# Kernel tuning notes

Hardware: AMD Instinct MI355X
Metric: run time of the kernel (lower is better)

Reference implementation:

```python
import jax, jax.numpy as jnp
import numpy as np

N = 25000      # nodes
E = 400000     # edges (avg degree 16)
MUL = 32       # multiplicity of each irrep block
NSC = 8        # num_edge_scalar_attr
HID = 64       # radial_neurons
WNUM = 4 * MUL # tp.weight_numel (4 uvu paths x mul 32)
NUM_NEIGH = 16.0
INV_SQRT3 = 1.0 / np.sqrt(3.0)   # component-normalized CG for 1o x 1o -> 0e


def setup_inputs() -> dict:
    key = jax.random.key(0)
    ks = jax.random.split(key, 13)
    return {
        'node_input': jax.random.normal(ks[0], (N, 4 * MUL), jnp.float32),
        'node_attr_input': jax.random.normal(ks[1], (N, 1), jnp.float32),
        'node_attr_output': jax.random.normal(ks[2], (N, 1), jnp.float32),
        'edge_src': jax.random.randint(ks[3], (E,), 0, N),
        'edge_dst': jax.random.randint(ks[4], (E,), 0, N),
        'edge_attr': jax.random.normal(ks[5], (E, 4), jnp.float32),
        'edge_scalar_attr': jax.random.normal(ks[6], (E, NSC), jnp.float32),
        # lin1: FCTP(32x0e+32x1o, 1x0e, 32x0e+32x1o) -> two uvw weight blocks (mul2=1 squeezed)
        'w1_s': jax.random.normal(ks[7], (MUL, MUL), jnp.float32),
        'w1_v': jax.random.normal(ks[8], (MUL, MUL), jnp.float32),
        # radial FC net [8, 64, 128]
        'Wfc1': jax.random.normal(ks[9], (NSC, HID), jnp.float32),
        'Wfc2': jax.random.normal(ks[10], (HID, WNUM), jnp.float32),
        # lin2: FCTP(irreps_mid, 1x0e, 32x0e+32x1o): 2 scalar blocks -> 0e, 2 vector blocks -> 1o
        'w2_s': jax.random.normal(ks[11], (2, MUL, MUL), jnp.float32),
        'w2_v': jax.random.normal(ks[12], (2, MUL, MUL), jnp.float32),
    }


def reference(node_input, node_attr_input, node_attr_output, edge_src, edge_dst,
              edge_attr, edge_scalar_attr, w1_s, w1_v, Wfc1, Wfc2, w2_s, w2_v):
    n = node_input.shape[0]
    # split node features into 32x0e scalars and 32x1o vectors
    xs = node_input[:, :MUL]                      # [N, 32]
    xv = node_input[:, MUL:].reshape(n, MUL, 3)   # [N, 32, 3]
    a = node_attr_input[:, 0]                     # [N]

    # ---- lin1: FullyConnectedTensorProduct with 1x0e attr (per-path alpha = 1/sqrt(mul1*mul2))
    inv1 = 1.0 / np.sqrt(MUL * 1.0)
    xs1 = jnp.einsum('nu,n,uw->nw', xs, a, w1_s) * inv1
    xv1 = jnp.einsum('nui,n,uw->nwi', xv, a, w1_v) * inv1

    # ---- radial FC net (silu MLP, fan-in normalized)
    h = jax.nn.silu(edge_scalar_attr @ Wfc1 * (1.0 / np.sqrt(NSC)))
    w = (h @ Wfc2 * (1.0 / np.sqrt(HID))).reshape(-1, 4, MUL)  # [E, 4 paths, 32]

    # ---- gather source node features per edge
    es = xs1[edge_src]            # [E, 32]
    ev = xv1[edge_src]            # [E, 32, 3]
    ys = edge_attr[:, 0]          # [E]    (0e sh)
    yv = edge_attr[:, 1:4]        # [E, 3] (1o sh)

    # ---- CG tensor product, 4 uvu instructions with per-edge weights
    m0 = w[:, 0] * es * ys[:, None]                                   # 0e x 0e -> 0e
    m3 = w[:, 3] * jnp.einsum('eui,ei->eu', ev, yv) * INV_SQRT3       # 1o x 1o -> 0e
    m1 = w[:, 1][:, :, None] * es[:, :, None] * yv[:, None, :]        # 0e x 1o -> 1o
    m2 = w[:, 2][:, :, None] * ev * ys[:, None, None]                 # 1o x 0e -> 1o
    ne = m0.shape[0]
    edge_features = jnp.concatenate(
        [m0, m3, m1.reshape(ne, 3 * MUL), m2.reshape(ne, 3 * MUL)], axis=1)  # [E, 256]

    # ---- scatter-sum to destination nodes, divide by sqrt(num_neighbors)
    mid = jax.ops.segment_sum(edge_features, edge_dst, num_segments=n)
    mid = mid / np.sqrt(NUM_NEIGH)

    # ---- lin2: FCTP(irreps_mid, 1x0e, 32x0e+32x1o), element norm: alpha = 1/sqrt(2*mul)
    b = node_attr_output[:, 0]
    inv2 = 1.0 / np.sqrt(2.0 * MUL)
    s0 = mid[:, :MUL]
    s1 = mid[:, MUL:2 * MUL]
    v1 = mid[:, 2 * MUL:2 * MUL + 3 * MUL].reshape(n, MUL, 3)
    v2 = mid[:, 2 * MUL + 3 * MUL:].reshape(n, MUL, 3)
    out_s = (jnp.einsum('nu,n,uw->nw', s0, b, w2_s[0]) +
             jnp.einsum('nu,n,uw->nw', s1, b, w2_s[1])) * inv2
    out_v = (jnp.einsum('nui,n,uw->nwi', v1, b, w2_v[0]) +
             jnp.einsum('nui,n,uw->nwi', v2, b, w2_v[1])) * inv2
    return jnp.concatenate([out_s, out_v.reshape(n, 3 * MUL)], axis=1)  # [N, 128]
```

## Files before the change

kernel.cpp:

```cpp
#include <hip/hip_runtime.h>


typedef __attribute__((ext_vector_type(8))) short bf16x8;
typedef __attribute__((ext_vector_type(4))) float f32x4;

__device__ __forceinline__ unsigned bf16r(float x) {
    unsigned u = __float_as_uint(x);
    return (u + 0x7fffu + ((u >> 16) & 1u)) >> 16;
}
__device__ __forceinline__ float bflo(unsigned p) { return __uint_as_float(p << 16); }
__device__ __forceinline__ float bfhi(unsigned p) { return __uint_as_float(p & 0xffff0000u); }

__global__ __launch_bounds__(256) void prep_kernel(
    const float* __restrict__ Wfc1, const float* __restrict__ Wfc2,
    float* __restrict__ W1s, float* __restrict__ W2T, unsigned short* __restrict__ W2Tb)
{
    int t = blockIdx.x * 256 + threadIdx.x;
    const float inv_sqrt_nsc = 0.35355339059327373f;
    if (t < 8 * 64) W1s[t] = Wfc1[t] * inv_sqrt_nsc;
    if (t < 64 * 128) {
        int r = t >> 7, c = t & 127;
        float v = Wfc2[t] * 0.125f;
        W2T[c * 64 + r] = v;
        W2Tb[c * 64 + r] = (unsigned short)bf16r(v);
    }
}

__global__ __launch_bounds__(256) void node_in_kernel(
    const float* __restrict__ node_input, const float* __restrict__ attr_in,
    const float* __restrict__ w1s, const float* __restrict__ w1v,
    float* __restrict__ xsv1, int n_nodes)
{
    __shared__ float sWs[1024], sWv[1024], srow[2][128];
    for (int k = threadIdx.x; k < 1024; k += 256) { sWs[k] = w1s[k]; sWv[k] = w1v[k]; }
    int j = threadIdx.x & 127;
    int half = threadIdx.x >> 7;
    int w = 0, i = 0;
    if (j >= 32) { int jj = j - 32; w = jj / 3; i = jj - 3 * w; }
    const float inv1 = 0.17677669529663687f;
    for (int base = blockIdx.x * 2; base < n_nodes; base += gridDim.x * 2) {
        int n = base + half;
        __syncthreads();
        if (n < n_nodes) srow[half][j] = node_input[(size_t)n * 128 + j];
        __syncthreads();
        if (n < n_nodes) {
            float acc = 0.0f;
            if (j < 32) {
                #pragma unroll
                for (int u = 0; u < 32; u++) acc += srow[half][u] * sWs[u * 32 + j];
            } else {
                #pragma unroll
                for (int u = 0; u < 32; u++) acc += srow[half][32 + 3 * u + i] * sWv[u * 32 + w];
            }
            xsv1[(size_t)n * 128 + j] = acc * (attr_in[n] * inv1);
        }
    }
}

__global__ __launch_bounds__(256) void count_kernel(
    const int* __restrict__ edst, int* __restrict__ counts, int n_edges)
{
    int e = blockIdx.x * 256 + threadIdx.x;
    if (e < n_edges) atomicAdd(&counts[edst[e]], 1);
}

__global__ __launch_bounds__(1024) void scan_kernel(
    const int* __restrict__ counts, int* __restrict__ offs, int* __restrict__ cursor, int n)
{
    __shared__ int part[1024];
    int tid = threadIdx.x;
    int chunk = (n + 1023) / 1024;
    int begin = tid * chunk;
    int end = begin + chunk; if (end > n) end = n;
    int s = 0;
    for (int i = begin; i < end; i++) s += counts[i];
    part[tid] = s;
    __syncthreads();
    for (int off = 1; off < 1024; off <<= 1) {
        int v = (tid >= off) ? part[tid - off] : 0;
        __syncthreads();
        part[tid] += v;
        __syncthreads();
    }
    int base = (tid == 0) ? 0 : part[tid - 1];
    for (int i = begin; i < end; i++) {
        offs[i] = base; cursor[i] = base;
        base += counts[i];
    }
    if (tid == 1023) offs[n] = part[1023];
}

__global__ __launch_bounds__(256) void scatter_kernel(
    const int* __restrict__ edst, const int* __restrict__ esrc,
    const float* __restrict__ eattr, const float* __restrict__ escal,
    int* __restrict__ cursor,
    int* __restrict__ esrc_s, float4* __restrict__ eattr_s, float4* __restrict__ escal_s,
    int n_edges)
{
    int e = blockIdx.x * 256 + threadIdx.x;
    if (e < n_edges) {
        int d = edst[e];
        int p = atomicAdd(&cursor[d], 1);
        esrc_s[p] = esrc[e];
        eattr_s[p] = *reinterpret_cast<const float4*>(eattr + (size_t)e * 4);
        escal_s[2 * (size_t)p]     = *reinterpret_cast<const float4*>(escal + (size_t)e * 8);
        escal_s[2 * (size_t)p + 1] = *reinterpret_cast<const float4*>(escal + (size_t)e * 8 + 4);
    }
}

#define TPW 8
__global__ __launch_bounds__(256) void edge_mlp_v4(
    const float4* __restrict__ escal_s,
    const float* __restrict__ W1s, const unsigned short* __restrict__ W2Tb,
    unsigned short* __restrict__ wbuf, int n_edges, int nrt)
{
    int tid = threadIdx.x;
    int wv = tid >> 6, l = tid & 63;
    int lm = l & 15, lk = l >> 4;
    int k0 = lk * 8;
    int rt0 = (blockIdx.x * 4 + wv) * TPW;

    bf16x8 bf[8][2];
    #pragma unroll
    for (int t = 0; t < 8; t++) {
        int n = t * 16 + lm;
        bf[t][0] = *reinterpret_cast<const bf16x8*>(W2Tb + n * 64 + k0);
        bf[t][1] = *reinterpret_cast<const bf16x8*>(W2Tb + n * 64 + k0 + 32);
    }

    #pragma unroll 2
    for (int t8 = 0; t8 < TPW; t8++) {
        int rt = rt0 + t8;
        if (rt >= nrt) break;
        int kidx = rt * 16 + lm;

        float q[8];
        if (kidx < n_edges) {
            float4 qa = escal_s[2 * (size_t)kidx];
            float4 qb = escal_s[2 * (size_t)kidx + 1];
            q[0] = qa.x; q[1] = qa.y; q[2] = qa.z; q[3] = qa.w;
            q[4] = qb.x; q[5] = qb.y; q[6] = qb.z; q[7] = qb.w;
        } else {
            #pragma unroll
            for (int i = 0; i < 8; i++) q[i] = 0.f;
        }

        union Af { bf16x8 v; unsigned u[4]; };
        Af af0, af1;
        #pragma unroll
        for (int half = 0; half < 2; half++) {
            int kb = k0 + half * 32;
            float h[8];
            #pragma unroll
            for (int i = 0; i < 8; i++) h[i] = 0.f;
            #pragma unroll
            for (int in = 0; in < 8; in++) {
                float qi = q[in];
                float4 wa = *reinterpret_cast<const float4*>(W1s + in * 64 + kb);
                float4 wb = *reinterpret_cast<const float4*>(W1s + in * 64 + kb + 4);
                h[0] += qi * wa.x; h[1] += qi * wa.y; h[2] += qi * wa.z; h[3] += qi * wa.w;
                h[4] += qi * wb.x; h[5] += qi * wb.y; h[6] += qi * wb.z; h[7] += qi * wb.w;
            }
            unsigned* dst = half ? af1.u : af0.u;
            #pragma unroll
            for (int p = 0; p < 4; p++) {
                float s0 = h[2 * p], s1 = h[2 * p + 1];
                s0 = s0 / (1.0f + __expf(-s0));
                s1 = s1 / (1.0f + __expf(-s1));
                dst[p] = bf16r(s0) | (bf16r(s1) << 16);
            }
        }

        #pragma unroll
        for (int t = 0; t < 8; t++) {
            f32x4 a4 = {0.f, 0.f, 0.f, 0.f};
            a4 = __builtin_amdgcn_mfma_f32_16x16x32_bf16(af0.v, bf[t][0], a4, 0, 0, 0);
            a4 = __builtin_amdgcn_mfma_f32_16x16x32_bf16(af1.v, bf[t][1], a4, 0, 0, 0);
            unsigned s0 = bf16r(a4[0]) | (bf16r(a4[1]) << 16);
            unsigned s1 = bf16r(a4[2]) | (bf16r(a4[3]) << 16);
            *reinterpret_cast<uint2*>(wbuf + ((size_t)(rt * 8 + t) * 256) + l * 4) = make_uint2(s0, s1);
        }
    }
}

__global__ __launch_bounds__(256) void gather_node_kernel(
    const unsigned short* __restrict__ wbuf, const float* __restrict__ xsv1,
    const int* __restrict__ esrc_s, const float4* __restrict__ eattr_s,
    const int* __restrict__ offs, float* __restrict__ mid, int n_nodes)
{
    int tid = threadIdx.x;
    int wv = __builtin_amdgcn_readfirstlane(tid >> 6);
    int L = tid & 63;
    int n = blockIdx.x * 4 + wv;
    if (n >= n_nodes) return;
    int g = L >> 4;

    int be, fbase; bool six;
    if (g == 0)      { be = 2 * L;       fbase = 2 * L;      six = false; }
    else if (g == 1) { be = 2 * L - 32;  fbase = 6 * L - 32; six = true;  }
    else if (g == 2) { be = 6 * L - 160; fbase = 6 * L - 32; six = true;  }
    else             { be = 6 * L - 256; fbase = 2 * L - 64; six = false; }

    const int colpart = ((2 * L) >> 4) * 256 + (((2 * L) & 15) << 2);

    const float inv_sqrt3 = 0.5773502691896258f;
    float a0 = 0.f, a1 = 0.f, a2 = 0.f, a3 = 0.f, a4 = 0.f, a5 = 0.f;
    int start = offs[n], end = offs[n + 1];

    #pragma unroll 4
    for (int k = start; k < end; k++) {
        float4 ea = eattr_s[k];
        int epart = (k >> 4) * 2048 + (((k >> 2) & 3) << 6);
        int sel = k & 3;
        uint4 wq = *reinterpret_cast<const uint4*>(wbuf + (size_t)epart + colpart);
        unsigned ulo = (sel & 2) ? wq.y : wq.x;
        unsigned uhi = (sel & 2) ? wq.w : wq.z;
        float wlo = (sel & 1) ? bfhi(ulo) : bflo(ulo);
        float whi = (sel & 1) ? bfhi(uhi) : bflo(uhi);
        int src = esrc_s[k];
        const float* __restrict__ nb = xsv1 + (size_t)src * 128;
        if (g == 0) {
            float2 x0 = *reinterpret_cast<const float2*>(nb + be);
            a0 += wlo * x0.x * ea.x;
            a1 += whi * x0.y * ea.x;
        } else if (g == 1) {
            float2 x0 = *reinterpret_cast<const float2*>(nb + be);
            float b0 = wlo * x0.x, b1 = whi * x0.y;
            a0 += b0 * ea.y; a1 += b0 * ea.z; a2 += b0 * ea.w;
            a3 += b1 * ea.y; a4 += b1 * ea.z; a5 += b1 * ea.w;
        } else {
            float2 x0 = *reinterpret_cast<const float2*>(nb + be);
            float2 x1 = *reinterpret_cast<const float2*>(nb + be + 2);
            float2 x2 = *reinterpret_cast<const float2*>(nb + be + 4);
            if (g == 2) {
                float b0 = wlo * ea.x, b1 = whi * ea.x;
                a0 += b0 * x0.x; a1 += b0 * x0.y; a2 += b0 * x1.x;
                a3 += b1 * x1.y; a4 += b1 * x2.x; a5 += b1 * x2.y;
            } else {
                a0 += wlo * (x0.x * ea.y + x0.y * ea.z + x1.x * ea.w) * inv_sqrt3;
                a1 += whi * (x1.y * ea.y + x2.x * ea.z + x2.y * ea.w) * inv_sqrt3;
            }
        }
    }

    float* row = mid + (size_t)n * 256 + fbase;
    *reinterpret_cast<float2*>(row) = make_float2(a0, a1);
    if (six) {
        *reinterpret_cast<float2*>(row + 2) = make_float2(a2, a3);
        *reinterpret_cast<float2*>(row + 4) = make_float2(a4, a5);
    }
}

__global__ __launch_bounds__(256) void edge_kernel_atomic(
    const float* __restrict__ xsv1, const int* __restrict__ esrc, const int* __restrict__ edst,
    const float* __restrict__ eattr, const float* __restrict__ escal,
    const float* __restrict__ W1s, const float* __restrict__ W2T,
    float* __restrict__ mid, int n_edges)
{
    int e = blockIdx.x * 256 + threadIdx.x;
    if (e >= n_edges) return;
    const float4 qa = *reinterpret_cast<const float4*>(escal + (size_t)e * 8);
    const float4 qb = *reinterpret_cast<const float4*>(escal + (size_t)e * 8 + 4);
    float h[64];
    #pragma unroll
    for (int t = 0; t < 64; t++) {
        float acc = qa.x * W1s[t]       + qa.y * W1s[64 + t]
                  + qa.z * W1s[128 + t] + qa.w * W1s[192 + t]
                  + qb.x * W1s[256 + t] + qb.y * W1s[320 + t]
                  + qb.z * W1s[384 + t] + qb.w * W1s[448 + t];
        h[t] = acc / (1.0f + __expf(-acc));
    }
    int src = esrc[e], dst = edst[e];
    const float4 ea = *reinterpret_cast<const float4*>(eattr + (size_t)e * 4);
    const float ys = ea.x, yv0 = ea.y, yv1 = ea.z, yv2 = ea.w;
    const float* __restrict__ nb = xsv1 + (size_t)src * 128;
    float* __restrict__ op = mid + (size_t)dst * 256;
    const float inv_sqrt3 = 0.5773502691896258f;
    for (int u = 0; u < 32; u++) {
        float w0 = 0.f, w1 = 0.f, w2 = 0.f, w3 = 0.f;
        const float* __restrict__ r0 = W2T + (size_t)u * 64;
        const float* __restrict__ r1 = W2T + (size_t)(32 + u) * 64;
        const float* __restrict__ r2 = W2T + (size_t)(64 + u) * 64;
        const float* __restrict__ r3 = W2T + (size_t)(96 + u) * 64;
        #pragma unroll
        for (int t = 0; t < 64; t++) {
            float hv = h[t];
            w0 += hv * r0[t]; w1 += hv * r1[t]; w2 += hv * r2[t]; w3 += hv * r3[t];
        }
        float es  = nb[u];
        float ev0 = nb[32 + 3 * u], ev1 = nb[33 + 3 * u], ev2 = nb[34 + 3 * u];
        atomicAdd(op + u,      w0 * es * ys);
        atomicAdd(op + 32 + u, w3 * (ev0 * yv0 + ev1 * yv1 + ev2 * yv2) * inv_sqrt3);
        float a1 = w1 * es;
        atomicAdd(op + 64 + 3 * u, a1 * yv0);
        atomicAdd(op + 65 + 3 * u, a1 * yv1);
        atomicAdd(op + 66 + 3 * u, a1 * yv2);
        float a2 = w2 * ys;
        atomicAdd(op + 160 + 3 * u, a2 * ev0);
        atomicAdd(op + 161 + 3 * u, a2 * ev1);
        atomicAdd(op + 162 + 3 * u, a2 * ev2);
    }
}

__global__ __launch_bounds__(256) void node_out_kernel(
    const float* __restrict__ mid, const float* __restrict__ attr_out,
    const float* __restrict__ w2s, const float* __restrict__ w2v,
    float* __restrict__ out, int n_nodes)
{
    __shared__ float sS0[1024], sS1[1024], sV0[1024], sV1[1024];
    for (int k = threadIdx.x; k < 1024; k += 256) {
        sS0[k] = w2s[k]; sS1[k] = w2s[1024 + k];
        sV0[k] = w2v[k]; sV1[k] = w2v[1024 + k];
    }
    __syncthreads();
    int j = threadIdx.x & 127;
    int half = threadIdx.x >> 7;
    int w = 0, i = 0;
    if (j >= 32) { int jj = j - 32; w = jj / 3; i = jj - 3 * w; }
    const float scale = 0.125f * 0.25f;
    for (int base = blockIdx.x * 2; base < n_nodes; base += gridDim.x * 2) {
        int n = base + half;
        if (n >= n_nodes) continue;
        const float* __restrict__ mr = mid + (size_t)n * 256;
        float acc = 0.0f;
        if (j < 32) {
            #pragma unroll
            for (int u = 0; u < 32; u++)
                acc += mr[u] * sS0[u * 32 + j] + mr[32 + u] * sS1[u * 32 + j];
        } else {
            #pragma unroll
            for (int u = 0; u < 32; u++)
                acc += mr[64 + 3 * u + i] * sV0[u * 32 + w] + mr[160 + 3 * u + i] * sV1[u * 32 + w];
        }
        out[(size_t)n * 128 + j] = acc * (attr_out[n] * scale);
    }
}

extern "C" void kernel_launch(void* const* d_in, const int* in_sizes, int n_in,
                              void* d_out, int out_size, void* d_ws, size_t ws_size,
                              hipStream_t stream)
{
    const float* node_input = (const float*)d_in[0];
    const float* attr_in    = (const float*)d_in[1];
    const float* attr_out   = (const float*)d_in[2];
    const int*   esrc       = (const int*)d_in[3];
    const int*   edst       = (const int*)d_in[4];
    const float* eattr      = (const float*)d_in[5];
    const float* escal      = (const float*)d_in[6];
    const float* w1s        = (const float*)d_in[7];
    const float* w1v        = (const float*)d_in[8];
    const float* Wfc1       = (const float*)d_in[9];
    const float* Wfc2       = (const float*)d_in[10];
    const float* w2s        = (const float*)d_in[11];
    const float* w2v        = (const float*)d_in[12];
    float* out = (float*)d_out;

    int n_nodes = in_sizes[0] / 128;
    int n_edges = in_sizes[3];
    int nrt = (n_edges + 15) / 16;
    int nwave = (nrt + TPW - 1) / TPW;
    int nblk = (nwave + 3) / 4;

    char* p = (char*)d_ws;
    auto alloc = [&](size_t bytes, size_t align) -> void* {
        size_t a = (size_t)p; a = (a + align - 1) & ~(align - 1);
        p = (char*)a; void* r = (void*)p; p += bytes; return r;
    };
    float* xsv1 = (float*)alloc((size_t)n_nodes * 128 * 4, 16);
    float* W1s  = (float*)alloc(512 * 4, 16);
    float* W2T  = (float*)alloc(8192 * 4, 16);
    float* mid  = (float*)alloc((size_t)n_nodes * 256 * 4, 16);
    int* counts = (int*)alloc((size_t)n_nodes * 4, 16);
    int* offs   = (int*)alloc(((size_t)n_nodes + 1) * 4, 16);
    int* cursor = (int*)alloc((size_t)n_nodes * 4, 16);
    int* esrc_s = (int*)alloc((size_t)n_edges * 4, 16);
    float4* eattr_s = (float4*)alloc((size_t)n_edges * 16, 16);
    float4* escal_s = (float4*)alloc((size_t)n_edges * 32, 16);
    unsigned short* W2Tb = (unsigned short*)alloc(8192 * 2, 64);
    unsigned short* wbuf = (unsigned short*)alloc((size_t)nrt * 8 * 256 * 2, 64);
    size_t needed = (size_t)(p - (char*)d_ws);

    prep_kernel<<<32, 256, 0, stream>>>(Wfc1, Wfc2, W1s, W2T, W2Tb);
    node_in_kernel<<<2048, 256, 0, stream>>>(node_input, attr_in, w1s, w1v, xsv1, n_nodes);

    if (ws_size >= needed) {
        hipMemsetAsync(counts, 0, (size_t)n_nodes * sizeof(int), stream);
        count_kernel<<<(n_edges + 255) / 256, 256, 0, stream>>>(edst, counts, n_edges);
        scan_kernel<<<1, 1024, 0, stream>>>(counts, offs, cursor, n_nodes);
        scatter_kernel<<<(n_edges + 255) / 256, 256, 0, stream>>>(
            edst, esrc, eattr, escal, cursor, esrc_s, eattr_s, escal_s, n_edges);
        edge_mlp_v4<<<nblk, 256, 0, stream>>>(escal_s, W1s, W2Tb, wbuf, n_edges, nrt);
        gather_node_kernel<<<(n_nodes + 3) / 4, 256, 0, stream>>>(
            wbuf, xsv1, esrc_s, eattr_s, offs, mid, n_nodes);
        node_out_kernel<<<2048, 256, 0, stream>>>(mid, attr_out, w2s, w2v, out, n_nodes);
    } else {
        hipMemsetAsync(mid, 0, (size_t)n_nodes * 256 * sizeof(float), stream);
        edge_kernel_atomic<<<(n_edges + 255) / 256, 256, 0, stream>>>(
            xsv1, esrc, edst, eattr, escal, W1s, W2T, mid, n_edges);
        node_out_kernel<<<2048, 256, 0, stream>>>(mid, attr_out, w2s, w2v, out, n_nodes);
    }
}
```

Measured before the change: 289.0 us.

## Fuse gather with output linear and split scatter into index scatter plus permute

The node gather kernel now keeps the 256-wide mid row in shared memory and applies the lin2 weights (loaded into LDS per block) directly, writing the final output and removing the mid round trip and the separate node_out launch. The scatter step is split in two: an atomic pass that only writes edge indices, then a permute pass that reads edge data by index and writes sorted outputs coalesced. This adds an extra kernel launch and an elist buffer, and each gather block reloads 16KB of weights into LDS, which lowers occupancy.

```diff
diff --git a/kernel.cpp b/kernel.cpp
--- a/kernel.cpp
+++ b/kernel.cpp
@@ -91,20 +91,29 @@
 }
 
 __global__ __launch_bounds__(256) void scatter_kernel(
-    const int* __restrict__ edst, const int* __restrict__ esrc,
+    const int* __restrict__ edst, int* __restrict__ cursor,
+    int* __restrict__ elist, int n_edges)
+{
+    int e = blockIdx.x * 256 + threadIdx.x;
+    if (e < n_edges) {
+        int p = atomicAdd(&cursor[edst[e]], 1);
+        elist[p] = e;
+    }
+}
+
+__global__ __launch_bounds__(256) void permute_kernel(
+    const int* __restrict__ elist, const int* __restrict__ esrc,
     const float* __restrict__ eattr, const float* __restrict__ escal,
-    int* __restrict__ cursor,
     int* __restrict__ esrc_s, float4* __restrict__ eattr_s, float4* __restrict__ escal_s,
     int n_edges)
 {
-    int e = blockIdx.x * 256 + threadIdx.x;
-    if (e < n_edges) {
-        int d = edst[e];
-        int p = atomicAdd(&cursor[d], 1);
-        esrc_s[p] = esrc[e];
-        eattr_s[p] = *reinterpret_cast<const float4*>(eattr + (size_t)e * 4);
-        escal_s[2 * (size_t)p]     = *reinterpret_cast<const float4*>(escal + (size_t)e * 8);
-        escal_s[2 * (size_t)p + 1] = *reinterpret_cast<const float4*>(escal + (size_t)e * 8 + 4);
+    int k = blockIdx.x * 256 + threadIdx.x;
+    if (k < n_edges) {
+        int e = elist[k];
+        esrc_s[k] = esrc[e];
+        eattr_s[k] = *reinterpret_cast<const float4*>(eattr + (size_t)e * 4);
+        escal_s[2 * (size_t)k]     = *reinterpret_cast<const float4*>(escal + (size_t)e * 8);
+        escal_s[2 * (size_t)k + 1] = *reinterpret_cast<const float4*>(escal + (size_t)e * 8 + 4);
     }
 }
 
@@ -183,16 +192,22 @@
     }
 }
 
-__global__ __launch_bounds__(256) void gather_node_kernel(
+__global__ __launch_bounds__(256) void gather_out_kernel(
     const unsigned short* __restrict__ wbuf, const float* __restrict__ xsv1,
     const int* __restrict__ esrc_s, const float4* __restrict__ eattr_s,
-    const int* __restrict__ offs, float* __restrict__ mid, int n_nodes)
-{
+    const int* __restrict__ offs, const float* __restrict__ attr_out,
+    const float* __restrict__ w2s, const float* __restrict__ w2v,
+    float* __restrict__ out, int n_nodes)
+{
+    __shared__ float sW[4096];
+    __shared__ float smid[4][256];
+
     int tid = threadIdx.x;
+    for (int idx = tid; idx < 2048; idx += 256) { sW[idx] = w2s[idx]; sW[2048 + idx] = w2v[idx]; }
+
     int wv = __builtin_amdgcn_readfirstlane(tid >> 6);
     int L = tid & 63;
     int n = blockIdx.x * 4 + wv;
-    if (n >= n_nodes) return;
     int g = L >> 4;
 
     int be, fbase; bool six;
@@ -202,52 +217,75 @@
     else             { be = 6 * L - 256; fbase = 2 * L - 64; six = false; }
 
     const int colpart = ((2 * L) >> 4) * 256 + (((2 * L) & 15) << 2);
-
     const float inv_sqrt3 = 0.5773502691896258f;
     float a0 = 0.f, a1 = 0.f, a2 = 0.f, a3 = 0.f, a4 = 0.f, a5 = 0.f;
-    int start = offs[n], end = offs[n + 1];
-
-    #pragma unroll 4
-    for (int k = start; k < end; k++) {
-        float4 ea = eattr_s[k];
-        int epart = (k >> 4) * 2048 + (((k >> 2) & 3) << 6);
-        int sel = k & 3;
-        uint4 wq = *reinterpret_cast<const uint4*>(wbuf + (size_t)epart + colpart);
-        unsigned ulo = (sel & 2) ? wq.y : wq.x;
-        unsigned uhi = (sel & 2) ? wq.w : wq.z;
-        float wlo = (sel & 1) ? bfhi(ulo) : bflo(ulo);
-        float whi = (sel & 1) ? bfhi(uhi) : bflo(uhi);
-        int src = esrc_s[k];
-        const float* __restrict__ nb = xsv1 + (size_t)src * 128;
-        if (g == 0) {
-            float2 x0 = *reinterpret_cast<const float2*>(nb + be);
-            a0 += wlo * x0.x * ea.x;
-            a1 += whi * x0.y * ea.x;
-        } else if (g == 1) {
-            float2 x0 = *reinterpret_cast<const float2*>(nb + be);
-            float b0 = wlo * x0.x, b1 = whi * x0.y;
-            a0 += b0 * ea.y; a1 += b0 * ea.z; a2 += b0 * ea.w;
-            a3 += b1 * ea.y; a4 += b1 * ea.z; a5 += b1 * ea.w;
-        } else {
-            float2 x0 = *reinterpret_cast<const float2*>(nb + be);
-            float2 x1 = *reinterpret_cast<const float2*>(nb + be + 2);
-            float2 x2 = *reinterpret_cast<const float2*>(nb + be + 4);
-            if (g == 2) {
-                float b0 = wlo * ea.x, b1 = whi * ea.x;
-                a0 += b0 * x0.x; a1 += b0 * x0.y; a2 += b0 * x1.x;
-                a3 += b1 * x1.y; a4 += b1 * x2.x; a5 += b1 * x2.y;
+
+    if (n < n_nodes) {
+        int start = offs[n], end = offs[n + 1];
+        #pragma unroll 4
+        for (int k = start; k < end; k++) {
+            float4 ea = eattr_s[k];
+            int epart = (k >> 4) * 2048 + (((k >> 2) & 3) << 6);
+            int sel = k & 3;
+            uint4 wq = *reinterpret_cast<const uint4*>(wbuf + (size_t)epart + colpart);
+            unsigned ulo = (sel & 2) ? wq.y : wq.x;
+            unsigned uhi = (sel & 2) ? wq.w : wq.z;
+            float wlo = (sel & 1) ? bfhi(ulo) : bflo(ulo);
+            float whi = (sel & 1) ? bfhi(uhi) : bflo(uhi);
+            int src = esrc_s[k];
+            const float* __restrict__ nb = xsv1 + (size_t)src * 128;
+            if (g == 0) {
+                float2 x0 = *reinterpret_cast<const float2*>(nb + be);
+                a0 += wlo * x0.x * ea.x;
+                a1 += whi * x0.y * ea.x;
+            } else if (g == 1) {
+                float2 x0 = *reinterpret_cast<const float2*>(nb + be);
+                float b0 = wlo * x0.x, b1 = whi * x0.y;
+                a0 += b0 * ea.y; a1 += b0 * ea.z; a2 += b0 * ea.w;
+                a3 += b1 * ea.y; a4 += b1 * ea.z; a5 += b1 * ea.w;
             } else {
-                a0 += wlo * (x0.x * ea.y + x0.y * ea.z + x1.x * ea.w) * inv_sqrt3;
-                a1 += whi * (x1.y * ea.y + x2.x * ea.z + x2.y * ea.w) * inv_sqrt3;
+                float2 x0 = *reinterpret_cast<const float2*>(nb + be);
+                float2 x1 = *reinterpret_cast<const float2*>(nb + be + 2);
+                float2 x2 = *reinterpret_cast<const float2*>(nb + be + 4);
+                if (g == 2) {
+                    float b0 = wlo * ea.x, b1 = whi * ea.x;
+                    a0 += b0 * x0.x; a1 += b0 * x0.y; a2 += b0 * x1.x;
+                    a3 += b1 * x1.y; a4 += b1 * x2.x; a5 += b1 * x2.y;
+                } else {
+                    a0 += wlo * (x0.x * ea.y + x0.y * ea.z + x1.x * ea.w) * inv_sqrt3;
+                    a1 += whi * (x1.y * ea.y + x2.x * ea.z + x2.y * ea.w) * inv_sqrt3;
+                }
             }
         }
     }
 
-    float* row = mid + (size_t)n * 256 + fbase;
-    *reinterpret_cast<float2*>(row) = make_float2(a0, a1);
-    if (six) {
-        *reinterpret_cast<float2*>(row + 2) = make_float2(a2, a3);
-        *reinterpret_cast<float2*>(row + 4) = make_float2(a4, a5);
+    float* row = &smid[wv][fbase];
+    row[0] = a0; row[1] = a1;
+    if (six) { row[2] = a2; row[3] = a3; row[4] = a4; row[5] = a5; }
+    __syncthreads();
+
+    int h = tid >> 7, j = tid & 127;
+    int tw = 0, ti = 0;
+    if (j >= 32) { int jj = j - 32; tw = jj / 3; ti = jj - 3 * tw; }
+    #pragma unroll
+    for (int it = 0; it < 2; it++) {
+        int ln = 2 * it + h;
+        int nn = blockIdx.x * 4 + ln;
+        if (nn < n_nodes) {
+            const float* __restrict__ sm = smid[ln];
+            float o = 0.0f;
+            if (j < 32) {
+                #pragma unroll
+                for (int u = 0; u < 32; u++)
+                    o += sm[u] * sW[u * 32 + j] + sm[32 + u] * sW[1024 + u * 32 + j];
+            } else {
+                #pragma unroll
+                for (int u = 0; u < 32; u++)
+                    o += sm[64 + 3 * u + ti] * sW[2048 + u * 32 + tw]
+                       + sm[160 + 3 * u + ti] * sW[3072 + u * 32 + tw];
+            }
+            out[(size_t)nn * 128 + j] = o * (attr_out[nn] * 0.03125f);
+        }
     }
 }
 
@@ -373,6 +411,7 @@
     int* counts = (int*)alloc((size_t)n_nodes * 4, 16);
     int* offs   = (int*)alloc(((size_t)n_nodes + 1) * 4, 16);
     int* cursor = (int*)alloc((size_t)n_nodes * 4, 16);
+    int* elist  = (int*)alloc((size_t)n_edges * 4, 16);
     int* esrc_s = (int*)alloc((size_t)n_edges * 4, 16);
     float4* eattr_s = (float4*)alloc((size_t)n_edges * 16, 16);
     float4* escal_s = (float4*)alloc((size_t)n_edges * 32, 16);
@@ -387,12 +426,12 @@
         hipMemsetAsync(counts, 0, (size_t)n_nodes * sizeof(int), stream);
         count_kernel<<<(n_edges + 255) / 256, 256, 0, stream>>>(edst, counts, n_edges);
         scan_kernel<<<1, 1024, 0, stream>>>(counts, offs, cursor, n_nodes);
-        scatter_kernel<<<(n_edges + 255) / 256, 256, 0, stream>>>(
-            edst, esrc, eattr, escal, cursor, esrc_s, eattr_s, escal_s, n_edges);
+        scatter_kernel<<<(n_edges + 255) / 256, 256, 0, stream>>>(edst, cursor, elist, n_edges);
+        permute_kernel<<<(n_edges + 255) / 256, 256, 0, stream>>>(
+            elist, esrc, eattr, escal, esrc_s, eattr_s, escal_s, n_edges);
         edge_mlp_v4<<<nblk, 256, 0, stream>>>(escal_s, W1s, W2Tb, wbuf, n_edges, nrt);
-        gather_node_kernel<<<(n_nodes + 3) / 4, 256, 0, stream>>>(
-            wbuf, xsv1, esrc_s, eattr_s, offs, mid, n_nodes);
-        node_out_kernel<<<2048, 256, 0, stream>>>(mid, attr_out, w2s, w2v, out, n_nodes);
+        gather_out_kernel<<<(n_nodes + 3) / 4, 256, 0, stream>>>(
+            wbuf, xsv1, esrc_s, eattr_s, offs, attr_out, w2s, w2v, out, n_nodes);
     } else {
         hipMemsetAsync(mid, 0, (size_t)n_nodes * 256 * sizeof(float), stream);
         edge_kernel_atomic<<<(n_edges + 255) / 256, 256, 0, stream>>>(
```

Result: no change. 285.9 us (-1.1%).
